# Performance work log

Measured on AMD Instinct MI355X. Metric: run time of the kernel, lower is better.

Reference implementation:

```python
import jax, jax.numpy as jnp
import numpy as np

NT, NH, NW = 16, 16, 16
HEADS, DIM_HEAD = 8, 64
DIM = 512
DEPTH = 4
EPS = 1e-5


def _layernorm(x, g, b):
    mu = jnp.mean(x, axis=-1, keepdims=True)
    var = jnp.mean(jnp.square(x - mu), axis=-1, keepdims=True)
    return (x - mu) * jax.lax.rsqrt(var + EPS) * g + b


def setup_inputs() -> dict:
    key = jax.random.key(0)
    ks = jax.random.split(key, 4)
    n = NT * NH * NW
    inner = HEADS * DIM_HEAD
    x = jax.random.normal(ks[0], (8, n, DIM), dtype=jnp.float32)
    Wqkv = jax.random.normal(ks[1], (DEPTH, DIM, 3 * inner), dtype=jnp.float32) * (DIM ** -0.5)
    Wout = jax.random.normal(ks[2], (DEPTH, inner, DIM), dtype=jnp.float32) * (inner ** -0.5)
    bout = jnp.zeros((DEPTH, DIM), dtype=jnp.float32)
    gamma = jnp.ones((DEPTH, DIM), dtype=jnp.float32)
    beta = jnp.zeros((DEPTH, DIM), dtype=jnp.float32)
    return {"x": x, "Wqkv": Wqkv, "Wout": Wout, "bout": bout, "gamma": gamma, "beta": beta}


def _fda_layer(x, Wqkv, Wout, bout, g, bb):
    b, n, d = x.shape
    hs = HEADS // 2
    s = NH * NW
    scale = DIM_HEAD ** -0.5
    y = _layernorm(x, g, bb)
    qkv = y @ Wqkv  # (b, n, 3*inner)
    q, k, v = jnp.split(qkv, 3, axis=-1)
    # b n (h d) -> b h n d
    def to_heads(t):
        return t.reshape(b, n, HEADS, DIM_HEAD).transpose(0, 2, 1, 3)
    q, k, v = to_heads(q), to_heads(k), to_heads(v)
    # spatial branch: first half of heads, view n as (t, s)
    qs = q[:, :hs].reshape(b, hs, NT, s, DIM_HEAD)
    ks = k[:, :hs].reshape(b, hs, NT, s, DIM_HEAD)
    vs = v[:, :hs].reshape(b, hs, NT, s, DIM_HEAD)
    sp_dots = jnp.einsum('bhtid,bhtjd->bhtij', qs, ks) * scale
    sp_attn = jax.nn.softmax(sp_dots, axis=-1)
    sp_out = jnp.einsum('bhtij,bhtjd->bhtid', sp_attn, vs)  # (b,hs,nt,s,dh)
    # temporal branch: second half of heads, view n as (s, t)
    qt = q[:, hs:].reshape(b, hs, s, NT, DIM_HEAD)
    kt = k[:, hs:].reshape(b, hs, s, NT, DIM_HEAD)
    vt = v[:, hs:].reshape(b, hs, s, NT, DIM_HEAD)
    tp_dots = jnp.einsum('bhsid,bhsjd->bhsij', qt, kt) * scale
    tp_attn = jax.nn.softmax(tp_dots, axis=-1)
    tp_out = jnp.einsum('bhsij,bhsjd->bhsid', tp_attn, vt)  # (b,hs,s,nt,dh)
    out = jnp.concatenate([sp_out.reshape(b, hs, n, DIM_HEAD),
                           tp_out.reshape(b, hs, n, DIM_HEAD)], axis=1)  # (b,h,n,dh)
    out = out.transpose(0, 2, 1, 3).reshape(b, n, HEADS * DIM_HEAD)
    return out @ Wout + bout


def reference(x, Wqkv, Wout, bout, gamma, beta):
    for l in range(DEPTH):
        x = _fda_layer(x, Wqkv[l], Wout[l], bout[l], gamma[l], beta[l]) + x
    return x
```

## Files before the change

### kernel.cpp

```cpp
#include <hip/hip_runtime.h>
#include <hip/hip_bf16.h>

typedef __bf16 bf16x8 __attribute__((ext_vector_type(8)));
typedef float f32x4 __attribute__((ext_vector_type(4)));

#define AS1(p) ((const __attribute__((address_space(1))) void*)(p))
#define AS3(p) ((__attribute__((address_space(3))) void*)(p))

__global__ __launch_bounds__(256) void transpose32(const float* __restrict__ W,
                                                   __bf16* __restrict__ WT,
                                                   int K, int N) {
  __shared__ float t[32][33];
  int l = blockIdx.z;
  int k0 = blockIdx.y * 32, n0 = blockIdx.x * 32;
  int tx = threadIdx.x & 31, ty = threadIdx.x >> 5;
  const float* src = W + ((size_t)l * K + k0) * N + n0;
#pragma unroll
  for (int i = 0; i < 32; i += 8) t[ty + i][tx] = src[(size_t)(ty + i) * N + tx];
  __syncthreads();
  __bf16* dst = WT + ((size_t)l * N + n0) * K + k0;
#pragma unroll
  for (int i = 0; i < 32; i += 8) dst[(size_t)(ty + i) * K + tx] = (__bf16)t[tx][ty + i];
}

__global__ __launch_bounds__(256) void ln_kernel(const float* __restrict__ x,
                                                 const float* __restrict__ gamma,
                                                 const float* __restrict__ beta,
                                                 __bf16* __restrict__ y) {
  int wave = threadIdx.x >> 6, lane = threadIdx.x & 63;
  size_t row = (size_t)blockIdx.x * 4 + wave;
  const float* xr = x + row * 512 + lane * 8;
  float4 v0 = *(const float4*)xr;
  float4 v1 = *(const float4*)(xr + 4);
  float s = v0.x + v0.y + v0.z + v0.w + v1.x + v1.y + v1.z + v1.w;
  float ss = v0.x * v0.x + v0.y * v0.y + v0.z * v0.z + v0.w * v0.w +
             v1.x * v1.x + v1.y * v1.y + v1.z * v1.z + v1.w * v1.w;
#pragma unroll
  for (int m = 1; m < 64; m <<= 1) {
    s += __shfl_xor(s, m);
    ss += __shfl_xor(ss, m);
  }
  float mean = s * (1.f / 512.f);
  float var = ss * (1.f / 512.f) - mean * mean;
  float rstd = rsqrtf(var + 1e-5f);
  const float* gp = gamma + lane * 8;
  const float* bp = beta + lane * 8;
  float4 g0 = *(const float4*)gp, g1 = *(const float4*)(gp + 4);
  float4 b0 = *(const float4*)bp, b1 = *(const float4*)(bp + 4);
  bf16x8 o;
  o[0] = (__bf16)((v0.x - mean) * rstd * g0.x + b0.x);
  o[1] = (__bf16)((v0.y - mean) * rstd * g0.y + b0.y);
  o[2] = (__bf16)((v0.z - mean) * rstd * g0.z + b0.z);
  o[3] = (__bf16)((v0.w - mean) * rstd * g0.w + b0.w);
  o[4] = (__bf16)((v1.x - mean) * rstd * g1.x + b1.x);
  o[5] = (__bf16)((v1.y - mean) * rstd * g1.y + b1.y);
  o[6] = (__bf16)((v1.z - mean) * rstd * g1.z + b1.z);
  o[7] = (__bf16)((v1.w - mean) * rstd * g1.w + b1.w);
  *(bf16x8*)(y + row * 512 + lane * 8) = o;
}

#define STAGE_PART(kt_, part_)                                                   \
  {                                                                              \
    const __bf16* gb_ = ((part_) < 2) ? Abase : Bbase;                           \
    int rowoff_ = ((part_)&1) * 128;                                             \
    const __bf16* g0_ = gb_ + (size_t)(rowoff_ + r0s) * 512 + (kt_)*64 + s0 * 8; \
    const __bf16* g1_ = gb_ + (size_t)(rowoff_ + r1s) * 512 + (kt_)*64 + s1 * 8; \
    char* lb_ = lds + (((kt_)&1) * 65536) + ((part_)*16384);                     \
    __builtin_amdgcn_global_load_lds(AS1(g0_), AS3(lb_ + ldsw0), 16, 0, 0);      \
    __builtin_amdgcn_global_load_lds(AS1(g1_), AS3(lb_ + ldsw1), 16, 0, 0);      \
  }

template <int NCOLS>
__global__ __launch_bounds__(512, 2) void gemm256(const __bf16* __restrict__ A,
                                                  const __bf16* __restrict__ BT,
                                                  __bf16* __restrict__ Cb) {
  extern __shared__ __attribute__((aligned(128))) char lds[];
  constexpr int NT = NCOLS / 256;
  int bid = blockIdx.x;
  int cpx = gridDim.x >> 3;
  int L = (bid & 7) * cpx + (bid >> 3);
  int tileM = L / NT, tileN = L - tileM * NT;
  int tid = threadIdx.x;
  int l = tid & 63, w = tid >> 6;
  int lm = l & 15, lh = l >> 4;
  int wave_m = w >> 2, wave_n = w & 3;
  const __bf16* Abase = A + (size_t)tileM * 256 * 512;
  const __bf16* Bbase = BT + (size_t)tileN * 256 * 512;
  int r0s = tid >> 3, s0 = (tid & 7) ^ (r0s & 7);
  int p1 = tid + 512;
  int r1s = p1 >> 3, s1 = (p1 & 7) ^ (r1s & 7);
  int ldsw0 = (w * 64) * 16, ldsw1 = (512 + w * 64) * 16;

  f32x4 acc[8][4];
#pragma unroll
  for (int m = 0; m < 8; ++m)
#pragma unroll
    for (int n = 0; n < 4; ++n) acc[m][n] = (f32x4){0.f, 0.f, 0.f, 0.f};

  int xorv = (lm & 7) << 4;
  int kb0 = (lh * 16) ^ xorv;
  int kb1 = (64 + lh * 16) ^ xorv;
  int arow = wave_m * 128 + lm;
  int brow = wave_n * 64 + lm;

  STAGE_PART(0, 0); STAGE_PART(0, 1); STAGE_PART(0, 2); STAGE_PART(0, 3);

  for (int kt = 0; kt < 8; ++kt) {
    char* sb = lds + (kt & 1) * 65536;
    if (kt < 7) {
      STAGE_PART(kt + 1, 0);
      asm volatile("s_waitcnt vmcnt(2)" ::: "memory");
    } else {
      asm volatile("s_waitcnt vmcnt(0)" ::: "memory");
    }
    __builtin_amdgcn_sched_barrier(0);
    __builtin_amdgcn_s_barrier();
    bf16x8 bfrag[4][2];
#pragma unroll
    for (int nf = 0; nf < 4; ++nf) {
      const char* bp = sb + 32768 + (brow + nf * 16) * 128;
      bfrag[nf][0] = *(const bf16x8*)(bp + kb0);
      bfrag[nf][1] = *(const bf16x8*)(bp + kb1);
    }
#pragma unroll
    for (int ph = 0; ph < 4; ++ph) {
      bf16x8 af[2][2];
#pragma unroll
      for (int m = 0; m < 2; ++m) {
        const char* ap = sb + (arow + (ph * 2 + m) * 16) * 128;
        af[m][0] = *(const bf16x8*)(ap + kb0);
        af[m][1] = *(const bf16x8*)(ap + kb1);
      }
      if (ph == 0 && kt < 7) STAGE_PART(kt + 1, 1);
      if (ph == 1 && kt < 7) STAGE_PART(kt + 1, 2);
      if (ph == 2 && kt < 7) STAGE_PART(kt + 1, 3);
      __builtin_amdgcn_s_setprio(1);
#pragma unroll
      for (int m = 0; m < 2; ++m)
#pragma unroll
        for (int nf = 0; nf < 4; ++nf) {
          acc[ph * 2 + m][nf] = __builtin_amdgcn_mfma_f32_16x16x32_bf16(
              af[m][0], bfrag[nf][0], acc[ph * 2 + m][nf], 0, 0, 0);
          acc[ph * 2 + m][nf] = __builtin_amdgcn_mfma_f32_16x16x32_bf16(
              af[m][1], bfrag[nf][1], acc[ph * 2 + m][nf], 0, 0, 0);
        }
      __builtin_amdgcn_s_setprio(0);
    }
    __builtin_amdgcn_s_barrier();
  }

  int crow = tileM * 256 + wave_m * 128 + lh * 4;
  int ccol = tileN * 256 + wave_n * 64 + lm;
#pragma unroll
  for (int mf = 0; mf < 8; ++mf)
#pragma unroll
    for (int nf = 0; nf < 4; ++nf) {
      int col = ccol + nf * 16;
#pragma unroll
      for (int r = 0; r < 4; ++r) {
        size_t idx = (size_t)(crow + mf * 16 + r) * NCOLS + col;
        Cb[idx] = (__bf16)acc[mf][nf][r];
      }
    }
}

#define STAGE128(kt_, part_)                                                    \
  {                                                                             \
    const __bf16* gb_ = ((part_) == 0) ? Abase : Bbase;                         \
    const __bf16* g0_ = gb_ + (size_t)r0s * 512 + (kt_)*64 + s0 * 8;            \
    const __bf16* g1_ = gb_ + (size_t)r1s * 512 + (kt_)*64 + s1 * 8;            \
    char* lb_ = lds + (((kt_)&1) * 32768) + ((part_)*16384);                    \
    __builtin_amdgcn_global_load_lds(AS1(g0_), AS3(lb_ + ldsw0), 16, 0, 0);     \
    __builtin_amdgcn_global_load_lds(AS1(g1_), AS3(lb_ + ldsw1), 16, 0, 0);     \
  }

__global__ __launch_bounds__(512, 4) void gemm128res(const __bf16* __restrict__ A,
                                                     const __bf16* __restrict__ BT,
                                                     float* Cf,
                                                     const float* __restrict__ bias,
                                                     const float* Resid) {
  extern __shared__ __attribute__((aligned(128))) char lds[];
  constexpr int NCOLS = 512;
  constexpr int NT = 4;
  int bid = blockIdx.x;
  int cpx = gridDim.x >> 3;
  int L = (bid & 7) * cpx + (bid >> 3);
  int tileM = L / NT, tileN = L - tileM * NT;
  int tid = threadIdx.x;
  int l = tid & 63, w = tid >> 6;
  int lm = l & 15, lh = l >> 4;
  int wave_m = w >> 2, wave_n = w & 3;
  const __bf16* Abase = A + (size_t)tileM * 128 * 512;
  const __bf16* Bbase = BT + (size_t)tileN * 128 * 512;
  int r0s = tid >> 3, s0 = (tid & 7) ^ (r0s & 7);
  int p1 = tid + 512;
  int r1s = p1 >> 3, s1 = (p1 & 7) ^ (r1s & 7);
  int ldsw0 = (w * 64) * 16, ldsw1 = 8192 + (w * 64) * 16;

  f32x4 acc[4][2];
#pragma unroll
  for (int m = 0; m < 4; ++m)
#pragma unroll
    for (int n = 0; n < 2; ++n) acc[m][n] = (f32x4){0.f, 0.f, 0.f, 0.f};

  int xorv = (lm & 7) << 4;
  int kb0 = (lh * 16) ^ xorv;
  int kb1 = (64 + lh * 16) ^ xorv;
  int arow = wave_m * 64 + lm;
  int brow = wave_n * 32 + lm;

  STAGE128(0, 0); STAGE128(0, 1);

  for (int kt = 0; kt < 8; ++kt) {
    char* sb = lds + (kt & 1) * 32768;
    if (kt < 7) {
      STAGE128(kt + 1, 0);
      asm volatile("s_waitcnt vmcnt(2)" ::: "memory");
    } else {
      asm volatile("s_waitcnt vmcnt(0)" ::: "memory");
    }
    __builtin_amdgcn_sched_barrier(0);
    __builtin_amdgcn_s_barrier();
    bf16x8 bfrag[2][2];
#pragma unroll
    for (int nf = 0; nf < 2; ++nf) {
      const char* bp = sb + 16384 + (brow + nf * 16) * 128;
      bfrag[nf][0] = *(const bf16x8*)(bp + kb0);
      bfrag[nf][1] = *(const bf16x8*)(bp + kb1);
    }
    bf16x8 af[4][2];
#pragma unroll
    for (int mf = 0; mf < 4; ++mf) {
      const char* ap = sb + (arow + mf * 16) * 128;
      af[mf][0] = *(const bf16x8*)(ap + kb0);
      af[mf][1] = *(const bf16x8*)(ap + kb1);
    }
    if (kt < 7) STAGE128(kt + 1, 1);
    __builtin_amdgcn_s_setprio(1);
#pragma unroll
    for (int mf = 0; mf < 4; ++mf)
#pragma unroll
      for (int nf = 0; nf < 2; ++nf) {
        acc[mf][nf] = __builtin_amdgcn_mfma_f32_16x16x32_bf16(af[mf][0], bfrag[nf][0],
                                                              acc[mf][nf], 0, 0, 0);
        acc[mf][nf] = __builtin_amdgcn_mfma_f32_16x16x32_bf16(af[mf][1], bfrag[nf][1],
                                                              acc[mf][nf], 0, 0, 0);
      }
    __builtin_amdgcn_s_setprio(0);
    __builtin_amdgcn_s_barrier();
  }

  float* lf = (float*)(lds + w * 2560);
  int crow0 = tileM * 128 + wave_m * 64;
  int ccol0 = tileN * 128 + wave_n * 32;
  int erow = l >> 2;
  int ecl = (l & 3) * 8;
  float4 ba = *(const float4*)(bias + ccol0 + ecl);
  float4 bb = *(const float4*)(bias + ccol0 + ecl + 4);
#pragma unroll
  for (int mf = 0; mf < 4; ++mf) {
#pragma unroll
    for (int nf = 0; nf < 2; ++nf)
#pragma unroll
      for (int r = 0; r < 4; ++r)
        lf[(lh * 4 + r) * 40 + nf * 16 + lm] = acc[mf][nf][r];
    size_t rowg = (size_t)(crow0 + mf * 16 + erow);
    const float* rp = Resid + rowg * NCOLS + ccol0 + ecl;
    float* cp = Cf + rowg * NCOLS + ccol0 + ecl;
    float4 a0 = *(float4*)&lf[erow * 40 + ecl];
    float4 a1 = *(float4*)&lf[erow * 40 + ecl + 4];
    float4 r0 = *(const float4*)rp;
    float4 r1 = *(const float4*)(rp + 4);
    float4 o0, o1;
    o0.x = a0.x + ba.x + r0.x; o0.y = a0.y + ba.y + r0.y;
    o0.z = a0.z + ba.z + r0.z; o0.w = a0.w + ba.w + r0.w;
    o1.x = a1.x + bb.x + r1.x; o1.y = a1.y + bb.y + r1.y;
    o1.z = a1.z + bb.z + r1.z; o1.w = a1.w + bb.w + r1.w;
    *(float4*)cp = o0;
    *(float4*)(cp + 4) = o1;
  }
}

__global__ __launch_bounds__(256) void attn_spatial(const __bf16* __restrict__ qkv,
                                                    __bf16* __restrict__ attn_out) {
  __shared__ __attribute__((aligned(16))) __bf16 VT[64 * 256];
  __shared__ __attribute__((aligned(16))) __bf16 P[4][4096];
  int bid = blockIdx.x;
  int b = bid >> 6;
  int rem = bid & 63;
  int h = rem >> 4;
  int t = rem & 15;
  int tid = threadIdx.x;
  int w = tid >> 6, l = tid & 63;
  size_t nbase = (size_t)b * 4096 + t * 256;
#pragma unroll
  for (int i = 0; i < 8; i++) {
    int idx = tid + i * 256;
    int key = idx >> 3, dseg = idx & 7;
    bf16x8 v = *(const bf16x8*)(qkv + (nbase + key) * 1536 + 1024 + h * 64 + dseg * 8);
#pragma unroll
    for (int d2 = 0; d2 < 8; d2++) {
      int dh = dseg * 8 + d2;
      VT[dh * 256 + (((key >> 3) ^ (dh & 7)) << 3) + (key & 7)] = v[d2];
    }
  }
  __syncthreads();
  int lm = l & 15, lh = l >> 4;
  for (int it = 0; it < 4; ++it) {
    int qbase = it * 64 + w * 16;
    const __bf16* qp = qkv + (nbase + qbase + lm) * 1536 + h * 64 + lh * 8;
    bf16x8 aq0 = *(const bf16x8*)qp;
    bf16x8 aq1 = *(const bf16x8*)(qp + 32);
    f32x4 sa[16];
#pragma unroll
    for (int tn = 0; tn < 16; ++tn) {
      const __bf16* kp = qkv + (nbase + tn * 16 + lm) * 1536 + 512 + h * 64 + lh * 8;
      bf16x8 bk0 = *(const bf16x8*)kp;
      bf16x8 bk1 = *(const bf16x8*)(kp + 32);
      f32x4 z = {0.f, 0.f, 0.f, 0.f};
      z = __builtin_amdgcn_mfma_f32_16x16x32_bf16(aq0, bk0, z, 0, 0, 0);
      sa[tn] = __builtin_amdgcn_mfma_f32_16x16x32_bf16(aq1, bk1, z, 0, 0, 0);
    }
    float rmax[4] = {-1e30f, -1e30f, -1e30f, -1e30f};
#pragma unroll
    for (int tn = 0; tn < 16; ++tn)
#pragma unroll
      for (int r = 0; r < 4; ++r) {
        sa[tn][r] *= 0.125f;
        rmax[r] = fmaxf(rmax[r], sa[tn][r]);
      }
#pragma unroll
    for (int m = 1; m < 16; m <<= 1)
#pragma unroll
      for (int r = 0; r < 4; ++r) rmax[r] = fmaxf(rmax[r], __shfl_xor(rmax[r], m));
    float rsum[4] = {0.f, 0.f, 0.f, 0.f};
#pragma unroll
    for (int tn = 0; tn < 16; ++tn)
#pragma unroll
      for (int r = 0; r < 4; ++r) {
        float e = __expf(sa[tn][r] - rmax[r]);
        sa[tn][r] = e;
        rsum[r] += e;
      }
#pragma unroll
    for (int m = 1; m < 16; m <<= 1)
#pragma unroll
      for (int r = 0; r < 4; ++r) rsum[r] += __shfl_xor(rsum[r], m);
    float rinv[4];
#pragma unroll
    for (int r = 0; r < 4; ++r) rinv[r] = 1.f / rsum[r];
#pragma unroll
    for (int tn = 0; tn < 16; ++tn)
#pragma unroll
      for (int r = 0; r < 4; ++r) {
        int row = lh * 4 + r;
        int col = tn * 16 + lm;
        P[w][row * 256 + ((((col >> 3)) ^ (row & 7)) << 3) + (col & 7)] =
            (__bf16)(sa[tn][r] * rinv[r]);
      }
    f32x4 oa[4];
#pragma unroll
    for (int nt = 0; nt < 4; ++nt) oa[nt] = (f32x4){0.f, 0.f, 0.f, 0.f};
#pragma unroll
    for (int kc = 0; kc < 8; ++kc) {
      bf16x8 pa = *(const bf16x8*)&P[w][lm * 256 + (((kc * 4 + lh) ^ (lm & 7)) << 3)];
#pragma unroll
      for (int nt = 0; nt < 4; ++nt) {
        int dh = nt * 16 + lm;
        bf16x8 bv = *(const bf16x8*)&VT[dh * 256 + (((kc * 4 + lh) ^ (dh & 7)) << 3)];
        oa[nt] = __builtin_amdgcn_mfma_f32_16x16x32_bf16(pa, bv, oa[nt], 0, 0, 0);
      }
    }
#pragma unroll
    for (int nt = 0; nt < 4; ++nt)
#pragma unroll
      for (int r = 0; r < 4; ++r) {
        size_t row = nbase + qbase + lh * 4 + r;
        attn_out[row * 512 + h * 64 + nt * 16 + lm] = (__bf16)oa[nt][r];
      }
  }
}

__global__ __launch_bounds__(256) void attn_temporal(const __bf16* __restrict__ qkv,
                                                     __bf16* __restrict__ attn_out) {
  __shared__ __attribute__((aligned(16))) __bf16 VT[4][64 * 40];
  __shared__ __attribute__((aligned(16))) __bf16 P[4][16 * 40];
  int tid = threadIdx.x;
  {
    float4 z4 = {0.f, 0.f, 0.f, 0.f};
#pragma unroll
    for (int i = 0; i < 5; ++i) ((float4*)&VT[0][0])[tid + i * 256] = z4;
    if (tid < 64) ((float4*)&P[0][0])[tid + 256] = z4;
    ((float4*)&P[0][0])[tid] = z4;
  }
  __syncthreads();
  int bid = blockIdx.x;
  int b = bid >> 8;
  int rem = bid & 255;
  int h = 4 + (rem >> 6);
  int g = rem & 63;
  int w = tid >> 6, l = tid & 63;
  int lm = l & 15, lh = l >> 4;
  int sid = g * 4 + w;
  size_t n0 = (size_t)b * 4096 + sid * 16;

  const __bf16* qp = qkv + (n0 + lm) * 1536 + h * 64 + lh * 8;
  bf16x8 aq0 = *(const bf16x8*)qp;
  bf16x8 aq1 = *(const bf16x8*)(qp + 32);
  const __bf16* kp = qp + 512;
  bf16x8 bk0 = *(const bf16x8*)kp;
  bf16x8 bk1 = *(const bf16x8*)(kp + 32);
  int kk = l >> 2;
  int dh0 = (l & 3) * 8;
  const __bf16* vp = qkv + (n0 + kk) * 1536 + 1024 + h * 64 + dh0;
  bf16x8 vr0 = *(const bf16x8*)vp;
  bf16x8 vr1 = *(const bf16x8*)(vp + 32);

  f32x4 s4 = {0.f, 0.f, 0.f, 0.f};
  s4 = __builtin_amdgcn_mfma_f32_16x16x32_bf16(aq0, bk0, s4, 0, 0, 0);
  s4 = __builtin_amdgcn_mfma_f32_16x16x32_bf16(aq1, bk1, s4, 0, 0, 0);

#pragma unroll
  for (int d2 = 0; d2 < 8; ++d2) VT[w][(dh0 + d2) * 40 + kk] = vr0[d2];
#pragma unroll
  for (int d2 = 0; d2 < 8; ++d2) VT[w][(dh0 + 32 + d2) * 40 + kk] = vr1[d2];

  float e[4];
  float rmax[4];
#pragma unroll
  for (int r = 0; r < 4; ++r) {
    e[r] = s4[r] * 0.125f;
    rmax[r] = e[r];
  }
#pragma unroll
  for (int m = 1; m < 16; m <<= 1)
#pragma unroll
    for (int r = 0; r < 4; ++r) rmax[r] = fmaxf(rmax[r], __shfl_xor(rmax[r], m));
  float rsum[4];
#pragma unroll
  for (int r = 0; r < 4; ++r) {
    e[r] = __expf(e[r] - rmax[r]);
    rsum[r] = e[r];
  }
#pragma unroll
  for (int m = 1; m < 16; m <<= 1)
#pragma unroll
    for (int r = 0; r < 4; ++r) rsum[r] += __shfl_xor(rsum[r], m);
#pragma unroll
  for (int r = 0; r < 4; ++r)
    P[w][(lh * 4 + r) * 40 + lm] = (__bf16)(e[r] / rsum[r]);

  asm volatile("s_waitcnt lgkmcnt(0)" ::: "memory");
  __builtin_amdgcn_sched_barrier(0);

  bf16x8 pa = *(const bf16x8*)&P[w][lm * 40 + lh * 8];
#pragma unroll
  for (int nt = 0; nt < 4; ++nt) {
    bf16x8 bv = *(const bf16x8*)&VT[w][(nt * 16 + lm) * 40 + lh * 8];
    f32x4 oa = {0.f, 0.f, 0.f, 0.f};
    oa = __builtin_amdgcn_mfma_f32_16x16x32_bf16(pa, bv, oa, 0, 0, 0);
#pragma unroll
    for (int r = 0; r < 4; ++r)
      attn_out[(n0 + lh * 4 + r) * 512 + h * 64 + nt * 16 + lm] = (__bf16)oa[r];
  }
}

extern "C" void kernel_launch(void* const* d_in, const int* in_sizes, int n_in,
                              void* d_out, int out_size, void* d_ws, size_t ws_size,
                              hipStream_t stream) {
  const float* x = (const float*)d_in[0];
  const float* Wqkv = (const float*)d_in[1];
  const float* Wout = (const float*)d_in[2];
  const float* bout = (const float*)d_in[3];
  const float* gamma = (const float*)d_in[4];
  const float* beta = (const float*)d_in[5];
  float* out = (float*)d_out;

  const size_t OFF_WOUT = 6291456;
  const size_t OFF_Y = OFF_WOUT + 2097152;
  const size_t OFF_QKV = OFF_Y + 33554432;
  const size_t NEEDED = OFF_QKV + 100663296;
  if (ws_size < NEEDED) return;
  char* ws = (char*)d_ws;
  __bf16* WqkvT = (__bf16*)ws;
  __bf16* WoutT = (__bf16*)(ws + OFF_WOUT);
  __bf16* ybuf = (__bf16*)(ws + OFF_Y);
  __bf16* qkv = (__bf16*)(ws + OFF_QKV);

  hipFuncSetAttribute((const void*)gemm256<1536>,
                      hipFuncAttributeMaxDynamicSharedMemorySize, 131072);
  hipFuncSetAttribute((const void*)gemm128res,
                      hipFuncAttributeMaxDynamicSharedMemorySize, 65536);

  transpose32<<<dim3(48, 16, 4), 256, 0, stream>>>(Wqkv, WqkvT, 512, 1536);
  transpose32<<<dim3(16, 16, 4), 256, 0, stream>>>(Wout, WoutT, 512, 512);

  for (int layer = 0; layer < 4; ++layer) {
    const float* src = (layer == 0) ? x : out;
    ln_kernel<<<8192, 256, 0, stream>>>(src, gamma + layer * 512, beta + layer * 512, ybuf);
    gemm256<1536><<<768, 512, 131072, stream>>>(
        ybuf, WqkvT + (size_t)layer * 1536 * 512, qkv);
    attn_spatial<<<512, 256, 0, stream>>>(qkv, ybuf);
    attn_temporal<<<2048, 256, 0, stream>>>(qkv, ybuf);
    gemm128res<<<1024, 512, 65536, stream>>>(
        ybuf, WoutT + (size_t)layer * 512 * 512, out, bout + layer * 512, src);
  }
}
```

Baseline: 662.5 us.

## Stage gemm256 epilogue through LDS and add a single-buffered variant for odd layers

The QKV GEMM epilogue now writes the accumulators into a padded per-wave LDS tile and reads them back as 16-byte rows. That replaces scattered 2-byte global stores with coalesced vector stores. A new single-buffered gemm256_sb kernel is also added, launched with 72 KB of LDS and launch bounds for 4 blocks per CU, and it is used only on odd layers. This looks like an A/B experiment. The stricter launch bound may force register spills of the 128-float accumulator, and the single buffer serialises loads with MFMA work.

```diff
diff --git a/kernel.cpp b/kernel.cpp
--- a/kernel.cpp
+++ b/kernel.cpp
@@ -58,6 +58,29 @@
   o[7] = (__bf16)((v1.w - mean) * rstd * g1.w + b1.w);
   *(bf16x8*)(y + row * 512 + lane * 8) = o;
 }
+
+#define GEMM256_EPILOGUE()                                                      \
+  __syncthreads();                                                              \
+  __bf16* lw = (__bf16*)(lds + w * 9216);                                       \
+  int crow0 = tileM * 256 + wave_m * 128;                                       \
+  int ccol = tileN * 256 + wave_n * 64 + (l & 7) * 8;                           \
+  _Pragma("unroll") for (int half = 0; half < 2; ++half) {                      \
+    _Pragma("unroll") for (int m2 = 0; m2 < 4; ++m2) {                          \
+      int mf = half * 4 + m2;                                                   \
+      _Pragma("unroll") for (int nf = 0; nf < 4; ++nf)                          \
+        _Pragma("unroll") for (int r = 0; r < 4; ++r)                           \
+          lw[(m2 * 16 + lh * 4 + r) * 72 + nf * 16 + lm] = (__bf16)acc[mf][nf][r]; \
+    }                                                                           \
+    asm volatile("s_waitcnt lgkmcnt(0)" ::: "memory");                          \
+    __builtin_amdgcn_sched_barrier(0);                                          \
+    _Pragma("unroll") for (int p = 0; p < 8; ++p) {                             \
+      int lrow = p * 8 + (l >> 3);                                              \
+      bf16x8 v = *(const bf16x8*)&lw[lrow * 72 + (l & 7) * 8];                  \
+      *(bf16x8*)&Cb[(size_t)(crow0 + half * 64 + lrow) * NCOLS + ccol] = v;     \
+    }                                                                           \
+    asm volatile("s_waitcnt lgkmcnt(0)" ::: "memory");                          \
+    __builtin_amdgcn_sched_barrier(0);                                          \
+  }
 
 #define STAGE_PART(kt_, part_)                                                   \
   {                                                                              \
@@ -149,19 +172,101 @@
     __builtin_amdgcn_s_barrier();
   }
 
-  int crow = tileM * 256 + wave_m * 128 + lh * 4;
-  int ccol = tileN * 256 + wave_n * 64 + lm;
-#pragma unroll
-  for (int mf = 0; mf < 8; ++mf)
+  GEMM256_EPILOGUE()
+}
+
+#define STAGE_SB(kt_, part_)                                                     \
+  {                                                                              \
+    const __bf16* gb_ = ((part_) < 2) ? Abase : Bbase;                           \
+    int rowoff_ = ((part_)&1) * 128;                                             \
+    const __bf16* g0_ = gb_ + (size_t)(rowoff_ + r0s) * 512 + (kt_)*64 + s0 * 8; \
+    const __bf16* g1_ = gb_ + (size_t)(rowoff_ + r1s) * 512 + (kt_)*64 + s1 * 8; \
+    char* lb_ = lds + ((part_)*16384);                                           \
+    __builtin_amdgcn_global_load_lds(AS1(g0_), AS3(lb_ + ldsw0), 16, 0, 0);      \
+    __builtin_amdgcn_global_load_lds(AS1(g1_), AS3(lb_ + ldsw1), 16, 0, 0);      \
+  }
+
+template <int NCOLS>
+__global__ __launch_bounds__(512, 4) void gemm256_sb(const __bf16* __restrict__ A,
+                                                     const __bf16* __restrict__ BT,
+                                                     __bf16* __restrict__ Cb) {
+  extern __shared__ __attribute__((aligned(128))) char lds[];
+  constexpr int NT = NCOLS / 256;
+  int bid = blockIdx.x;
+  int cpx = gridDim.x >> 3;
+  int L = (bid & 7) * cpx + (bid >> 3);
+  int tileM = L / NT, tileN = L - tileM * NT;
+  int tid = threadIdx.x;
+  int l = tid & 63, w = tid >> 6;
+  int lm = l & 15, lh = l >> 4;
+  int wave_m = w >> 2, wave_n = w & 3;
+  const __bf16* Abase = A + (size_t)tileM * 256 * 512;
+  const __bf16* Bbase = BT + (size_t)tileN * 256 * 512;
+  int r0s = tid >> 3, s0 = (tid & 7) ^ (r0s & 7);
+  int p1 = tid + 512;
+  int r1s = p1 >> 3, s1 = (p1 & 7) ^ (r1s & 7);
+  int ldsw0 = (w * 64) * 16, ldsw1 = (512 + w * 64) * 16;
+
+  f32x4 acc[8][4];
+#pragma unroll
+  for (int m = 0; m < 8; ++m)
+#pragma unroll
+    for (int n = 0; n < 4; ++n) acc[m][n] = (f32x4){0.f, 0.f, 0.f, 0.f};
+
+  int xorv = (lm & 7) << 4;
+  int kb0 = (lh * 16) ^ xorv;
+  int kb1 = (64 + lh * 16) ^ xorv;
+  int arow = wave_m * 128 + lm;
+  int brow = wave_n * 64 + lm;
+
+  STAGE_SB(0, 0); STAGE_SB(0, 1); STAGE_SB(0, 2); STAGE_SB(0, 3);
+  asm volatile("s_waitcnt vmcnt(0)" ::: "memory");
+  __builtin_amdgcn_sched_barrier(0);
+  __builtin_amdgcn_s_barrier();
+
+  for (int kt = 0; kt < 8; ++kt) {
+    const char* sb = lds;
+    bf16x8 bfrag[4][2];
 #pragma unroll
     for (int nf = 0; nf < 4; ++nf) {
-      int col = ccol + nf * 16;
-#pragma unroll
-      for (int r = 0; r < 4; ++r) {
-        size_t idx = (size_t)(crow + mf * 16 + r) * NCOLS + col;
-        Cb[idx] = (__bf16)acc[mf][nf][r];
-      }
-    }
+      const char* bp = sb + 32768 + (brow + nf * 16) * 128;
+      bfrag[nf][0] = *(const bf16x8*)(bp + kb0);
+      bfrag[nf][1] = *(const bf16x8*)(bp + kb1);
+    }
+#pragma unroll
+    for (int ph = 0; ph < 4; ++ph) {
+      bf16x8 af[2][2];
+#pragma unroll
+      for (int m = 0; m < 2; ++m) {
+        const char* ap = sb + (arow + (ph * 2 + m) * 16) * 128;
+        af[m][0] = *(const bf16x8*)(ap + kb0);
+        af[m][1] = *(const bf16x8*)(ap + kb1);
+      }
+      __builtin_amdgcn_s_setprio(1);
+#pragma unroll
+      for (int m = 0; m < 2; ++m)
+#pragma unroll
+        for (int nf = 0; nf < 4; ++nf) {
+          acc[ph * 2 + m][nf] = __builtin_amdgcn_mfma_f32_16x16x32_bf16(
+              af[m][0], bfrag[nf][0], acc[ph * 2 + m][nf], 0, 0, 0);
+          acc[ph * 2 + m][nf] = __builtin_amdgcn_mfma_f32_16x16x32_bf16(
+              af[m][1], bfrag[nf][1], acc[ph * 2 + m][nf], 0, 0, 0);
+        }
+      __builtin_amdgcn_s_setprio(0);
+    }
+    asm volatile("s_waitcnt lgkmcnt(0)" ::: "memory");
+    __builtin_amdgcn_sched_barrier(0);
+    __builtin_amdgcn_s_barrier();
+    if (kt < 7) {
+      STAGE_SB(kt + 1, 0); STAGE_SB(kt + 1, 1);
+      STAGE_SB(kt + 1, 2); STAGE_SB(kt + 1, 3);
+      asm volatile("s_waitcnt vmcnt(0)" ::: "memory");
+      __builtin_amdgcn_sched_barrier(0);
+      __builtin_amdgcn_s_barrier();
+    }
+  }
+
+  GEMM256_EPILOGUE()
 }
 
 #define STAGE128(kt_, part_)                                                    \
@@ -489,6 +594,8 @@
 
   hipFuncSetAttribute((const void*)gemm256<1536>,
                       hipFuncAttributeMaxDynamicSharedMemorySize, 131072);
+  hipFuncSetAttribute((const void*)gemm256_sb<1536>,
+                      hipFuncAttributeMaxDynamicSharedMemorySize, 73728);
   hipFuncSetAttribute((const void*)gemm128res,
                       hipFuncAttributeMaxDynamicSharedMemorySize, 65536);
 
@@ -498,8 +605,13 @@
   for (int layer = 0; layer < 4; ++layer) {
     const float* src = (layer == 0) ? x : out;
     ln_kernel<<<8192, 256, 0, stream>>>(src, gamma + layer * 512, beta + layer * 512, ybuf);
-    gemm256<1536><<<768, 512, 131072, stream>>>(
-        ybuf, WqkvT + (size_t)layer * 1536 * 512, qkv);
+    if (layer & 1) {
+      gemm256_sb<1536><<<768, 512, 73728, stream>>>(
+          ybuf, WqkvT + (size_t)layer * 1536 * 512, qkv);
+    } else {
+      gemm256<1536><<<768, 512, 131072, stream>>>(
+          ybuf, WqkvT + (size_t)layer * 1536 * 512, qkv);
+    }
     attn_spatial<<<512, 256, 0, stream>>>(qkv, ybuf);
     attn_temporal<<<2048, 256, 0, stream>>>(qkv, ybuf);
     gemm128res<<<1024, 512, 65536, stream>>>(
```

Result: slower. 1.232 ms (+85.9%).
